# Performance work log

Measured on AMD Instinct MI355X. Metric: run time of the kernel, lower is better.

Reference implementation:

```python
import jax, jax.numpy as jnp
import numpy as np

B, Ci, Cr, Hb, Wb = 2, 256, 128, 200, 200
Ca, NH, DH = 128, 8, 16          # attn_channels = min(256,128); 8 heads of dim 16
K = 100                           # max(16, int(0.5*W)), K < W so topk path is active
EPS = 1e-5


def ln(x, g, b):
    m = x.mean(-1, keepdims=True)
    v = ((x - m) ** 2).mean(-1, keepdims=True)
    return (x - m) / jnp.sqrt(v + EPS) * g + b


def setup_inputs() -> dict:
    key = jax.random.key(0)
    ks = jax.random.split(key, 16)
    def n(k, shape, s=0.02):
        return jax.random.normal(k, shape, dtype=jnp.float32) * s
    return dict(
        radar_features=jax.random.normal(ks[0], (B, Cr, Hb, Wb), dtype=jnp.float32),
        image_features=jax.random.normal(ks[1], (B, Ci, Hb, Wb), dtype=jnp.float32),
        img_proj_w=n(ks[2], (Ca, Ci)),
        rad_proj_w=n(ks[3], (Ca, Cr)),
        in_proj_w=n(ks[4], (3 * Ca, Ca)),
        in_proj_b=jnp.zeros((3 * Ca,), jnp.float32),
        out_proj_w=n(ks[5], (Ca, Ca)),
        out_proj_b=jnp.zeros((Ca,), jnp.float32),
        ln1q_g=jnp.ones((Ca,), jnp.float32), ln1q_b=jnp.zeros((Ca,), jnp.float32),
        ln1kv_g=jnp.ones((Ca,), jnp.float32), ln1kv_b=jnp.zeros((Ca,), jnp.float32),
        ln2_g=jnp.ones((Ca,), jnp.float32), ln2_b=jnp.zeros((Ca,), jnp.float32),
        ffn_w1=n(ks[6], (4 * Ca, Ca)), ffn_b1=jnp.zeros((4 * Ca,), jnp.float32),
        ffn_w2=n(ks[7], (Ca, 4 * Ca)), ffn_b2=jnp.zeros((Ca,), jnp.float32),
        score_w1=n(ks[8], (Ca // 2, 2 * Ca)), score_b1=jnp.zeros((Ca // 2,), jnp.float32),
        score_w2=n(ks[9], (1, Ca // 2)), score_b2=jnp.zeros((1,), jnp.float32),
        rad_delta_w=n(ks[10], (Cr, Ca)),
        gamma=jnp.full((1,), 0.5, jnp.float32),  # torch inits to 0; 0.5 so attn branch affects output
        gate_w=n(ks[11], (Cr, Cr + Ci)), gate_b=jnp.zeros((Cr,), jnp.float32),
        fuse_w=n(ks[12], (Cr + Ci, Cr + Ci, 3, 3)),
        bn_g=jnp.ones((Cr + Ci,), jnp.float32), bn_b=jnp.zeros((Cr + Ci,), jnp.float32),
    )


def reference(radar_features, image_features, img_proj_w, rad_proj_w, in_proj_w, in_proj_b,
              out_proj_w, out_proj_b, ln1q_g, ln1q_b, ln1kv_g, ln1kv_b, ln2_g, ln2_b,
              ffn_w1, ffn_b1, ffn_w2, ffn_b2, score_w1, score_b1, score_w2, score_b2,
              rad_delta_w, gamma, gate_w, gate_b, fuse_w, bn_g, bn_b):
    # 1x1 projections into attention space, then per-row sequences [B*H, W, Ca]
    img_seq = jnp.einsum('bchw,oc->bhwo', image_features, img_proj_w).reshape(B * Hb, Wb, Ca)
    rad_seq = jnp.einsum('bchw,oc->bhwo', radar_features, rad_proj_w).reshape(B * Hb, Wb, Ca)

    # progressive focus: score each image token per row, keep top-K as KV
    si = jnp.concatenate([jax.lax.stop_gradient(rad_seq), img_seq], axis=-1)
    h = jax.nn.relu(si @ score_w1.T + score_b1)
    score = (h @ score_w2.T + score_b2)[..., 0]            # [B*H, W]
    _, idx = jax.lax.top_k(score, K)                       # [B*H, K]
    img_kv = jnp.take_along_axis(img_seq, idx[:, :, None], axis=1)  # [B*H, K, Ca]

    # cross attention (pre-LN on q and kv, residual onto rad_seq)
    q = ln(rad_seq, ln1q_g, ln1q_b)
    kv = ln(img_kv, ln1kv_g, ln1kv_b)
    wq, wk, wv = in_proj_w[:Ca], in_proj_w[Ca:2 * Ca], in_proj_w[2 * Ca:]
    bq, bk, bv = in_proj_b[:Ca], in_proj_b[Ca:2 * Ca], in_proj_b[2 * Ca:]
    qh = (q @ wq.T + bq).reshape(B * Hb, Wb, NH, DH)
    kh = (kv @ wk.T + bk).reshape(B * Hb, K, NH, DH)
    vh = (kv @ wv.T + bv).reshape(B * Hb, K, NH, DH)
    att = jax.nn.softmax(jnp.einsum('nqhd,nkhd->nhqk', qh, kh) / jnp.sqrt(jnp.float32(DH)), axis=-1)
    o = jnp.einsum('nhqk,nkhd->nqhd', att, vh).reshape(B * Hb, Wb, Ca) @ out_proj_w.T + out_proj_b
    x = rad_seq + o
    x = x + (jax.nn.relu(ln(x, ln2_g, ln2_b) @ ffn_w1.T + ffn_b1) @ ffn_w2.T + ffn_b2)

    # back to BEV, project delta to radar channels
    delta = jnp.einsum('bhwc,oc->bohw', x.reshape(B, Hb, Wb, Ca), rad_delta_w)

    # cross-modal gate (1x1 conv + sigmoid) with range-decay mask
    gate_in = jnp.concatenate([radar_features, image_features], axis=1)
    gate = jax.nn.sigmoid(jnp.einsum('bchw,oc->bohw', gate_in, gate_w) + gate_b[None, :, None, None])
    y = jnp.arange(Hb, dtype=jnp.float32) / (Hb - 1)
    rmask = jnp.clip(1.0 - 0.7 * y, 0.3, None)[None, None, :, None]
    gate = gate * rmask

    radar_enhanced = radar_features + gamma * gate * delta

    # fuse: 3x3 conv + BatchNorm (batch stats, training mode) + ReLU
    fi = jnp.concatenate([radar_enhanced, image_features], axis=1)
    c = jax.lax.conv_general_dilated(fi, fuse_w, (1, 1), 'SAME',
                                     dimension_numbers=('NCHW', 'OIHW', 'NCHW'))
    m = c.mean((0, 2, 3), keepdims=True)
    v = ((c - m) ** 2).mean((0, 2, 3), keepdims=True)
    out = jax.nn.relu((c - m) / jnp.sqrt(v + EPS) * bn_g[None, :, None, None] + bn_b[None, :, None, None])
    return out
```

## Files before the change

### kernel.cpp

```cpp
#include <hip/hip_runtime.h>
#include <hip/hip_bf16.h>

#define EPSF 1e-5f

typedef unsigned short u16;
typedef unsigned int u32;
typedef __attribute__((ext_vector_type(8))) short short8v;
typedef __attribute__((ext_vector_type(4))) float f32x4;

__device__ float g_arena[84000000];
__device__ float g_stats[768];

__device__ __forceinline__ float wave_sum(float v) {
#pragma unroll
    for (int o = 32; o > 0; o >>= 1) v += __shfl_down(v, o, 64);
    return v;
}

__device__ __forceinline__ void gload16(const u16* g, u16* l) {
    __builtin_amdgcn_global_load_lds(
        (const __attribute__((address_space(1))) u32*)(g),
        (__attribute__((address_space(3))) u32*)(l),
        16, 0, 0);
}

__device__ __forceinline__ void bf_split(float v, u16& h, u16& l) {
    __hip_bfloat16 bh = __float2bfloat16(v);
    float hv = __bfloat162float(bh);
    __hip_bfloat16 bl = __float2bfloat16(v - hv);
    h = *reinterpret_cast<u16*>(&bh);
    l = *reinterpret_cast<u16*>(&bl);
}

__device__ __forceinline__ void store_split4(u16* ph, u16* pl, float4 v) {
    u16 h0, l0, h1, l1, h2, l2, h3, l3;
    bf_split(v.x, h0, l0); bf_split(v.y, h1, l1);
    bf_split(v.z, h2, l2); bf_split(v.w, h3, l3);
    *(ushort4*)ph = make_ushort4(h0, h1, h2, h3);
    *(ushort4*)pl = make_ushort4(l0, l1, l2, l3);
}

__global__ __launch_bounds__(256) void split_weights_kernel(
    const float* __restrict__ w_inproj, const float* __restrict__ w_outproj,
    const float* __restrict__ w_ffn1, const float* __restrict__ w_ffn2,
    const float* __restrict__ w_delta, const float* __restrict__ w_gate,
    const float* __restrict__ w_img, const float* __restrict__ w_rad,
    const float* __restrict__ w_sc1, const float* __restrict__ b_sc1,
    u16* __restrict__ wseg, float* __restrict__ bias_pad,
    float* __restrict__ zpage)
{
    int i = blockIdx.x * 256 + threadIdx.x;
    if (i >= 393408) return;
    if (i >= 393344) {
        zpage[i - 393344] = 0.f;
        return;
    }
    if (i >= 393216) {
        int l = i - 393216;
        bias_pad[l] = (l < 64) ? b_sc1[l] : 0.f;
        return;
    }
    float v; int base, numel, local;
    if (i < 49152)       { local = i;          base = 0;      numel = 49152; v = w_inproj[local]; }
    else if (i < 65536)  { local = i - 49152;  base = 98304;  numel = 16384; v = w_outproj[local]; }
    else if (i < 131072) { local = i - 65536;  base = 131072; numel = 65536; v = w_ffn1[local]; }
    else if (i < 196608) { local = i - 131072; base = 262144; numel = 65536; v = w_ffn2[local]; }
    else if (i < 212992) { local = i - 196608; base = 393216; numel = 16384; v = w_delta[local]; }
    else if (i < 262144) { local = i - 212992; base = 425984; numel = 49152; v = w_gate[local]; }
    else if (i < 360448) {
        local = i - 262144; base = 524288; numel = 98304;
        int oc = local / 384, c = local - oc * 384;
        if (oc < 128) v = (c < 128) ? w_rad[oc * 128 + c] : 0.f;
        else          v = (c >= 128) ? w_img[(oc - 128) * 256 + (c - 128)] : 0.f;
    } else {
        local = i - 360448; base = 720896; numel = 32768;
        int oc = local / 256, c = local - oc * 256;
        v = (oc < 64) ? w_sc1[oc * 256 + c] : 0.f;
    }
    u16 hh, ll;
    bf_split(v, hh, ll);
    wseg[base + local] = hh;
    wseg[base + numel + local] = ll;
}

template <int BMODE, int OMODE, bool RELU>
__global__ __launch_bounds__(256, (BMODE == 1) ? 3 : 2) void mfma_gemm_kernel(
    const u16* __restrict__ Ah, const u16* __restrict__ Al,
    const u16* __restrict__ bh, const u16* __restrict__ bl,
    const float* __restrict__ bf, int bstride,
    const float* __restrict__ bias, const float* __restrict__ resid, int rstride,
    float* __restrict__ outf, u16* __restrict__ outh,
    int K, int Nout, int P, const u16* __restrict__ zp)
{
    __shared__ alignas(16) u16 sAh[8192], sAl[8192], sBh[8192];
    __shared__ alignas(16) u16 sBl[(BMODE != 1) ? 8192 : 8];

    const int tid  = threadIdx.x;
    const int lane = tid & 63;
    const int wid  = tid >> 6;
    const int wrm  = wid >> 1;
    const int wcn  = wid & 1;
    const int p0   = blockIdx.x * 128;
    const int ocb  = blockIdx.y * 128;

    const int r0  = tid >> 3;
    const int cl  = tid & 7;
    const int swz = cl ^ (r0 & 7);

    f32x4 acc[4][4];
#pragma unroll
    for (int i = 0; i < 4; ++i)
#pragma unroll
        for (int j = 0; j < 4; ++j) acc[i][j] = (f32x4){0.f, 0.f, 0.f, 0.f};

    const int fr = lane & 15;
    const int fc = lane >> 4;

    for (int kk = 0; kk < K; kk += 64) {
        __syncthreads();
#pragma unroll
        for (int k = 0; k < 4; ++k) {
            int row = r0 + k * 32;
            int dlin = row * 64 + cl * 8;
            size_t ga = (size_t)(ocb + row) * K + kk + swz * 8;
            gload16(&Ah[ga], &sAh[dlin]);
            gload16(&Al[ga], &sAl[dlin]);
            int p = p0 + row;
            if (BMODE == 0) {
                size_t gb = (size_t)p * bstride + kk + swz * 8;
                const u16* bsh = (p < P) ? &bh[gb] : zp;
                const u16* bsl = (p < P) ? &bl[gb] : zp;
                gload16(bsh, &sBh[dlin]);
                gload16(bsl, &sBl[dlin]);
            } else if (BMODE == 1) {
                size_t gb = (size_t)p * bstride + kk + swz * 8;
                const u16* bsh = (p < P) ? &bh[gb] : zp;
                gload16(bsh, &sBh[dlin]);
            } else {
                int di = row * 64 + swz * 8;
                short8v vh8 = {0,0,0,0,0,0,0,0}, vl8 = {0,0,0,0,0,0,0,0};
                if (p < P) {
                    const float* src = bf + (size_t)p * bstride + kk + cl * 8;
                    float4 f0 = *(const float4*)(src);
                    float4 f1 = *(const float4*)(src + 4);
                    float fv[8] = {f0.x, f0.y, f0.z, f0.w, f1.x, f1.y, f1.z, f1.w};
#pragma unroll
                    for (int j = 0; j < 8; ++j) {
                        u16 hh, ll;
                        bf_split(fv[j], hh, ll);
                        vh8[j] = (short)hh;
                        vl8[j] = (short)ll;
                    }
                }
                *(short8v*)&sBh[di] = vh8;
                *(short8v*)&sBl[di] = vl8;
            }
        }
        __syncthreads();
#pragma unroll
        for (int h = 0; h < 2; ++h) {
            const int kc = h * 4 + fc;
            short8v bhf[4], blf[4];
#pragma unroll
            for (int nn = 0; nn < 4; ++nn) {
                int row = wcn * 64 + nn * 16 + fr;
                int idx = row * 64 + ((kc ^ (row & 7)) << 3);
                bhf[nn] = *(const short8v*)&sBh[idx];
                if (BMODE != 1) blf[nn] = *(const short8v*)&sBl[idx];
            }
#pragma unroll
            for (int mm = 0; mm < 4; ++mm) {
                int row = wrm * 64 + mm * 16 + fr;
                int idx = row * 64 + ((kc ^ (row & 7)) << 3);
                short8v ahf = *(const short8v*)&sAh[idx];
                short8v alf = *(const short8v*)&sAl[idx];
#pragma unroll
                for (int nn = 0; nn < 4; ++nn)
                    acc[mm][nn] = __builtin_amdgcn_mfma_f32_16x16x32_bf16(
                        ahf, bhf[nn], acc[mm][nn], 0, 0, 0);
                if (BMODE != 1) {
#pragma unroll
                    for (int nn = 0; nn < 4; ++nn)
                        acc[mm][nn] = __builtin_amdgcn_mfma_f32_16x16x32_bf16(
                            ahf, blf[nn], acc[mm][nn], 0, 0, 0);
                }
#pragma unroll
                for (int nn = 0; nn < 4; ++nn)
                    acc[mm][nn] = __builtin_amdgcn_mfma_f32_16x16x32_bf16(
                        alf, bhf[nn], acc[mm][nn], 0, 0, 0);
            }
        }
    }

#pragma unroll
    for (int mm = 0; mm < 4; ++mm) {
        int base = ocb + wrm * 64 + mm * 16 + fc * 4;
        float4 bv = {0.f, 0.f, 0.f, 0.f};
        if (bias) bv = *(const float4*)&bias[base];
#pragma unroll
        for (int nn = 0; nn < 4; ++nn) {
            int p = p0 + wcn * 64 + nn * 16 + fr;
            if (p < P) {
                size_t row = (size_t)p * Nout + base;
                float4 r;
                r.x = acc[mm][nn][0] + bv.x;
                r.y = acc[mm][nn][1] + bv.y;
                r.z = acc[mm][nn][2] + bv.z;
                r.w = acc[mm][nn][3] + bv.w;
                if (resid) {
                    float4 rr = *(const float4*)&resid[(size_t)p * rstride + base - ocb];
                    r.x += rr.x; r.y += rr.y; r.z += rr.z; r.w += rr.w;
                }
                if (RELU) {
                    r.x = fmaxf(r.x, 0.f); r.y = fmaxf(r.y, 0.f);
                    r.z = fmaxf(r.z, 0.f); r.w = fmaxf(r.w, 0.f);
                }
                if (OMODE == 0) {
                    *(float4*)&outf[row] = r;
                } else {
                    __hip_bfloat16 b0 = __float2bfloat16(r.x);
                    __hip_bfloat16 b1 = __float2bfloat16(r.y);
                    __hip_bfloat16 b2 = __float2bfloat16(r.z);
                    __hip_bfloat16 b3 = __float2bfloat16(r.w);
                    *(ushort4*)&outh[row] = make_ushort4(
                        *reinterpret_cast<u16*>(&b0), *reinterpret_cast<u16*>(&b1),
                        *reinterpret_cast<u16*>(&b2), *reinterpret_cast<u16*>(&b3));
                }
            }
        }
    }
}

__global__ __launch_bounds__(256) void score_reduce_kernel(
    const float* __restrict__ h, const float* __restrict__ w2,
    const float* __restrict__ b2, float* __restrict__ score)
{
    int p = blockIdx.x * 4 + (threadIdx.x >> 6);
    int l = threadIdx.x & 63;
    float v = h[(size_t)p * 128 + l] * w2[l];
    v = wave_sum(v);
    if (l == 0) score[p] = v + b2[0];
}

__global__ __launch_bounds__(256) void topk_kernel(
    const float* __restrict__ score, int* __restrict__ idx)
{
    __shared__ float s[200];
    const int n = blockIdx.x;
    const int t = threadIdx.x;
    if (t < 200) s[t] = score[(size_t)n * 200 + t];
    __syncthreads();
    if (t < 200) {
        float my = s[t];
        int cnt = 0;
        for (int j = 0; j < 200; j++) {
            float o = s[j];
            cnt += (o > my) || (o == my && j < t);
        }
        if (cnt < 100) idx[n * 100 + cnt] = t;
    }
}

__global__ __launch_bounds__(256) void ln_gather_kernel(
    const float* __restrict__ in, int stride, const int* __restrict__ gidx,
    const float* __restrict__ g, const float* __restrict__ bb,
    u16* __restrict__ oh, u16* __restrict__ ol)
{
    __shared__ float red[4];
    const int tid = threadIdx.x;
    const int grp = tid >> 7;
    const int t = tid & 127;
    const int r = blockIdx.x * 2 + grp;

    size_t src_row;
    if (gidx) src_row = (size_t)(r / 100) * 200 + gidx[r];
    else      src_row = (size_t)r;

    float x = in[src_row * stride + t];
    float s = wave_sum(x);
    if ((tid & 63) == 0) red[tid >> 6] = s;
    __syncthreads();
    float m = (red[grp * 2] + red[grp * 2 + 1]) * 0.0078125f;
    float d = x - m;
    float s2 = wave_sum(d * d);
    __syncthreads();
    if ((tid & 63) == 0) red[tid >> 6] = s2;
    __syncthreads();
    float var = (red[grp * 2] + red[grp * 2 + 1]) * 0.0078125f;
    float y = d * rsqrtf(var + EPSF) * g[t] + bb[t];
    u16 hh, ll;
    bf_split(y, hh, ll);
    oh[(size_t)r * 128 + t] = hh;
    ol[(size_t)r * 128 + t] = ll;
}

__global__ __launch_bounds__(256) void attention_kernel(
    const float* __restrict__ qh, const float* __restrict__ kvh,
    u16* __restrict__ o_hi, u16* __restrict__ o_lo)
{
    __shared__ float sk[100][16];
    __shared__ float sv[100][16];
    const int h = blockIdx.x;
    const int n = blockIdx.y;
    const int tid = threadIdx.x;

    for (int e = tid; e < 1600; e += 256) {
        int kk = e >> 4, d = e & 15;
        size_t src = ((size_t)n * 100 + kk) * 256 + h * 16 + d;
        sk[kk][d] = kvh[src];
        sv[kk][d] = kvh[src + 128];
    }
    __syncthreads();

    if (tid < 200) {
        const float* qp = &qh[((size_t)n * 200 + tid) * 128 + h * 16];
        float4 q0 = *(const float4*)(qp + 0);
        float4 q1 = *(const float4*)(qp + 4);
        float4 q2 = *(const float4*)(qp + 8);
        float4 q3 = *(const float4*)(qp + 12);

        float m = -INFINITY, l = 0.f;
        float4 a0 = {0,0,0,0}, a1 = {0,0,0,0}, a2 = {0,0,0,0}, a3 = {0,0,0,0};

        for (int kk = 0; kk < 100; kk++) {
            const float4* kp = (const float4*)&sk[kk][0];
            float s = q0.x*kp[0].x + q0.y*kp[0].y + q0.z*kp[0].z + q0.w*kp[0].w
                    + q1.x*kp[1].x + q1.y*kp[1].y + q1.z*kp[1].z + q1.w*kp[1].w
                    + q2.x*kp[2].x + q2.y*kp[2].y + q2.z*kp[2].z + q2.w*kp[2].w
                    + q3.x*kp[3].x + q3.y*kp[3].y + q3.z*kp[3].z + q3.w*kp[3].w;
            s *= 0.25f;
            float nm = fmaxf(m, s);
            float corr = __expf(m - nm);
            float pe = __expf(s - nm);
            l = l * corr + pe;
            const float4* vp = (const float4*)&sv[kk][0];
            float4 v0 = vp[0], v1 = vp[1], v2 = vp[2], v3 = vp[3];
            a0.x = a0.x * corr + pe * v0.x; a0.y = a0.y * corr + pe * v0.y;
            a0.z = a0.z * corr + pe * v0.z; a0.w = a0.w * corr + pe * v0.w;
            a1.x = a1.x * corr + pe * v1.x; a1.y = a1.y * corr + pe * v1.y;
            a1.z = a1.z * corr + pe * v1.z; a1.w = a1.w * corr + pe * v1.w;
            a2.x = a2.x * corr + pe * v2.x; a2.y = a2.y * corr + pe * v2.y;
            a2.z = a2.z * corr + pe * v2.z; a2.w = a2.w * corr + pe * v2.w;
            a3.x = a3.x * corr + pe * v3.x; a3.y = a3.y * corr + pe * v3.y;
            a3.z = a3.z * corr + pe * v3.z; a3.w = a3.w * corr + pe * v3.w;
            m = nm;
        }
        float inv = 1.f / l;
        a0.x *= inv; a0.y *= inv; a0.z *= inv; a0.w *= inv;
        a1.x *= inv; a1.y *= inv; a1.z *= inv; a1.w *= inv;
        a2.x *= inv; a2.y *= inv; a2.z *= inv; a2.w *= inv;
        a3.x *= inv; a3.y *= inv; a3.z *= inv; a3.w *= inv;
        size_t ob = ((size_t)n * 200 + tid) * 128 + h * 16;
        store_split4(&o_hi[ob + 0],  &o_lo[ob + 0],  a0);
        store_split4(&o_hi[ob + 4],  &o_lo[ob + 4],  a1);
        store_split4(&o_hi[ob + 8],  &o_lo[ob + 8],  a2);
        store_split4(&o_hi[ob + 12], &o_lo[ob + 12], a3);
    }
}

__global__ __launch_bounds__(256) void prep_weights_kernel(
    const float* __restrict__ fw, u16* __restrict__ wh, u16* __restrict__ wl)
{
    int idx = blockIdx.x * 256 + threadIdx.x;
    int oc = idx / 384;
    int ic = idx - oc * 384;
    const float* src = fw + (size_t)idx * 9;
    u16* dh = wh + (size_t)oc * 3456 + ic;
    u16* dl = wl + (size_t)oc * 3456 + ic;
#pragma unroll
    for (int s = 0; s < 9; ++s) {
        u16 hh, ll;
        bf_split(src[s], hh, ll);
        dh[(size_t)s * 384] = hh;
        dl[(size_t)s * 384] = ll;
    }
}

__global__ __launch_bounds__(256) void convert_nhwc_kernel(
    const float* __restrict__ radar, const float* __restrict__ image,
    u16* __restrict__ oh, u16* __restrict__ ol)
{
    int p = blockIdx.x * 256 + threadIdx.x;
    if (p >= 80000) return;
    int cg = blockIdx.y;
    int b = p >= 40000 ? 1 : 0;
    int hw = p - b * 40000;
    u16* ph = oh + (size_t)p * 384 + cg * 64;
    u16* pl = ol + (size_t)p * 384 + cg * 64;
#pragma unroll 1
    for (int g = 0; g < 8; ++g) {
        short8v vh, vl;
#pragma unroll
        for (int j = 0; j < 8; ++j) {
            int c = cg * 64 + g * 8 + j;
            float v = (c < 128)
                ? radar[((size_t)(b * 128 + c)) * 40000 + hw]
                : image[((size_t)(b * 256 + (c - 128))) * 40000 + hw];
            u16 hh, ll;
            bf_split(v, hh, ll);
            vh[j] = (short)hh;
            vl[j] = (short)ll;
        }
        *(short8v*)&ph[g * 8] = vh;
        *(short8v*)&pl[g * 8] = vl;
    }
}

__global__ __launch_bounds__(256) void enhance_fuse_kernel(
    const float* __restrict__ delta, const float* __restrict__ gatepre,
    const float* __restrict__ radar, const float* __restrict__ gamma_p,
    u16* __restrict__ nh)
{
    __shared__ float srad[64][136];
    const int tid = threadIdx.x;
    const int blk = blockIdx.x;
    const int b = blk >= 625 ? 1 : 0;
    const int hw0 = (blk - b * 625) * 64;
    const int p0 = b * 40000 + hw0;

#pragma unroll
    for (int i = 0; i < 32; ++i) {
        int e = tid + i * 256;
        int oc = e >> 6, pos = e & 63;
        srad[pos][oc] = radar[((size_t)(b * 128 + oc)) * 40000 + hw0 + pos];
    }
    __syncthreads();

    const float gmm = gamma_p[0];
    const int c4 = tid & 31;
    const int rr = tid >> 5;
#pragma unroll
    for (int j = 0; j < 8; ++j) {
        int pos = j * 8 + rr;
        int p = p0 + pos;
        int hw = hw0 + pos;
        int hrow = hw / 200;
        float rm = fmaxf(0.3f, 1.0f - 0.7f * ((float)hrow * (1.0f / 199.0f)));
        float4 dv = *(const float4*)&delta[(size_t)p * 128 + c4 * 4];
        float4 gv = *(const float4*)&gatepre[(size_t)p * 128 + c4 * 4];
        float4 rv = *(const float4*)&srad[pos][c4 * 4];
        float rx = rv.x + gmm * (1.f / (1.f + __expf(-gv.x))) * rm * dv.x;
        float ry = rv.y + gmm * (1.f / (1.f + __expf(-gv.y))) * rm * dv.y;
        float rz = rv.z + gmm * (1.f / (1.f + __expf(-gv.z))) * rm * dv.z;
        float rw = rv.w + gmm * (1.f / (1.f + __expf(-gv.w))) * rm * dv.w;
        __hip_bfloat16 b0 = __float2bfloat16(rx);
        __hip_bfloat16 b1 = __float2bfloat16(ry);
        __hip_bfloat16 b2 = __float2bfloat16(rz);
        __hip_bfloat16 b3 = __float2bfloat16(rw);
        *(ushort4*)&nh[(size_t)p * 384 + c4 * 4] = make_ushort4(
            *reinterpret_cast<u16*>(&b0), *reinterpret_cast<u16*>(&b1),
            *reinterpret_cast<u16*>(&b2), *reinterpret_cast<u16*>(&b3));
    }
}

__global__ __launch_bounds__(256, 3) void conv_mfma_kernel(
    const u16* __restrict__ nhwc_hi,
    const u16* __restrict__ wgt_hi,  const u16* __restrict__ wgt_lo,
    float* __restrict__ out, const u16* __restrict__ zp)
{
    __shared__ alignas(16) u16 sAh[8192], sAl[8192], sBh[8192];

    const int tid  = threadIdx.x;
    const int lane = tid & 63;
    const int wid  = tid >> 6;
    const int wrm  = wid >> 1;
    const int wcn  = wid & 1;
    const int hw0  = blockIdx.x * 128;
    const int b    = blockIdx.y;
    const int oc0  = blockIdx.z * 128;

    const int r0  = tid >> 3;
    const int cl  = tid & 7;
    const int swz = cl ^ (r0 & 7);

    const int y0 = hw0 / 200;
    const int x0 = hw0 - y0 * 200;

    f32x4 acc[4][4];
#pragma unroll
    for (int i = 0; i < 4; ++i)
#pragma unroll
        for (int j = 0; j < 4; ++j) acc[i][j] = (f32x4){0.f, 0.f, 0.f, 0.f};

    size_t abase[4];
#pragma unroll
    for (int k = 0; k < 4; ++k)
        abase[k] = (size_t)(oc0 + r0 + k * 32) * 3456 + swz * 8;

    const int fr = lane & 15;
    const int fc = lane >> 4;

    for (int s = 0; s < 9; ++s) {
        const int dy = s / 3 - 1;
        const int dx = s % 3 - 1;
        size_t bsrc[4];
        int bval[4];
#pragma unroll
        for (int k = 0; k < 4; ++k) {
            int row = r0 + k * 32;
            int hwo = hw0 + row;
            int xr  = x0 + row;
            int wrp = (xr >= 200) ? 1 : 0;
            int yy  = y0 + wrp + dy;
            int xx  = xr - wrp * 200 + dx;
            int v = (hwo < 40000) && ((unsigned)yy < 200u) && ((unsigned)xx < 200u);
            bval[k] = v;
            bsrc[k] = v ? ((size_t)(b * 40000 + yy * 200 + xx) * 384 + swz * 8) : 0;
        }
        const size_t wofs = (size_t)s * 384;

        for (int icb = 0; icb < 6; ++icb) {
            const int ic0 = icb * 64;
            __syncthreads();
#pragma unroll
            for (int k = 0; k < 4; ++k) {
                int dlin = (r0 + k * 32) * 64 + cl * 8;
                size_t ga = abase[k] + wofs + ic0;
                gload16(&wgt_hi[ga], &sAh[dlin]);
                gload16(&wgt_lo[ga], &sAl[dlin]);
                const u16* bs = bval[k] ? &nhwc_hi[bsrc[k] + ic0] : zp;
                gload16(bs, &sBh[dlin]);
            }
            __syncthreads();
#pragma unroll
            for (int h = 0; h < 2; ++h) {
                const int kc = h * 4 + fc;
                short8v bhf[4];
#pragma unroll
                for (int nn = 0; nn < 4; ++nn) {
                    int row = wcn * 64 + nn * 16 + fr;
                    int idx = row * 64 + ((kc ^ (row & 7)) << 3);
                    bhf[nn] = *(const short8v*)&sBh[idx];
                }
#pragma unroll
                for (int mm = 0; mm < 4; ++mm) {
                    int row = wrm * 64 + mm * 16 + fr;
                    int idx = row * 64 + ((kc ^ (row & 7)) << 3);
                    short8v ahf = *(const short8v*)&sAh[idx];
                    short8v alf = *(const short8v*)&sAl[idx];
#pragma unroll
                    for (int nn = 0; nn < 4; ++nn)
                        acc[mm][nn] = __builtin_amdgcn_mfma_f32_16x16x32_bf16(
                            ahf, bhf[nn], acc[mm][nn], 0, 0, 0);
#pragma unroll
                    for (int nn = 0; nn < 4; ++nn)
                        acc[mm][nn] = __builtin_amdgcn_mfma_f32_16x16x32_bf16(
                            alf, bhf[nn], acc[mm][nn], 0, 0, 0);
                }
            }
        }
    }

#pragma unroll
    for (int mm = 0; mm < 4; ++mm) {
        int oc = oc0 + wrm * 64 + mm * 16 + fc * 4;
#pragma unroll
        for (int nn = 0; nn < 4; ++nn) {
            int p = hw0 + wcn * 64 + nn * 16 + fr;
            if (p < 40000) {
                float* op = out + (size_t)(b * 384 + oc) * 40000 + p;
#pragma unroll
                for (int r = 0; r < 4; ++r)
                    op[(size_t)r * 40000] = acc[mm][nn][r];
            }
        }
    }
}

__global__ void zero_stats_kernel() {
    int i = blockIdx.x * 256 + threadIdx.x;
    if (i < 768) g_stats[i] = 0.f;
}

__global__ __launch_bounds__(256) void conv_stats_kernel(const float* __restrict__ out)
{
    const int c = blockIdx.x;
    const int chunk = blockIdx.y;
    float s1 = 0.f, s2 = 0.f;
#pragma unroll
    for (int b = 0; b < 2; ++b) {
        const float4* pp = (const float4*)(out + (size_t)(b * 384 + c) * 40000)
                         + (size_t)chunk * 2500;
        for (int i = threadIdx.x; i < 2500; i += 256) {
            float4 v = pp[i];
            s1 += v.x + v.y + v.z + v.w;
            s2 += v.x * v.x + v.y * v.y + v.z * v.z + v.w * v.w;
        }
    }
    s1 = wave_sum(s1);
    s2 = wave_sum(s2);
    __shared__ float r1[4], r2[4];
    if ((threadIdx.x & 63) == 0) {
        r1[threadIdx.x >> 6] = s1;
        r2[threadIdx.x >> 6] = s2;
    }
    __syncthreads();
    if (threadIdx.x == 0) {
        atomicAdd(&g_stats[c * 2],     r1[0] + r1[1] + r1[2] + r1[3]);
        atomicAdd(&g_stats[c * 2 + 1], r2[0] + r2[1] + r2[2] + r2[3]);
    }
}

__global__ __launch_bounds__(256) void bn_relu_kernel(
    float* __restrict__ out, const float* __restrict__ g,
    const float* __restrict__ bb)
{
    int i = blockIdx.x * 256 + threadIdx.x;
    int flat = i * 4;
    int oc = (flat / 40000) % 384;
    float m = g_stats[oc * 2] * (1.f / 80000.f);
    float v = g_stats[oc * 2 + 1] * (1.f / 80000.f) - m * m;
    float inv = rsqrtf(v + EPSF);
    float sc = g[oc] * inv;
    float sh = bb[oc] - m * sc;
    float4 c = ((float4*)out)[i];
    c.x = fmaxf(c.x * sc + sh, 0.f);
    c.y = fmaxf(c.y * sc + sh, 0.f);
    c.z = fmaxf(c.z * sc + sh, 0.f);
    c.w = fmaxf(c.w * sc + sh, 0.f);
    ((float4*)out)[i] = c;
}

extern "C" void kernel_launch(void* const* d_in, const int* in_sizes, int n_in,
                              void* d_out, int out_size, void* d_ws, size_t ws_size,
                              hipStream_t stream)
{
    (void)in_sizes; (void)n_in; (void)out_size; (void)d_ws; (void)ws_size;

    const float* radar      = (const float*)d_in[0];
    const float* image      = (const float*)d_in[1];
    const float* img_proj_w = (const float*)d_in[2];
    const float* rad_proj_w = (const float*)d_in[3];
    const float* in_proj_w  = (const float*)d_in[4];
    const float* in_proj_b  = (const float*)d_in[5];
    const float* out_proj_w = (const float*)d_in[6];
    const float* out_proj_b = (const float*)d_in[7];
    const float* ln1q_g     = (const float*)d_in[8];
    const float* ln1q_b     = (const float*)d_in[9];
    const float* ln1kv_g    = (const float*)d_in[10];
    const float* ln1kv_b    = (const float*)d_in[11];
    const float* ln2_g      = (const float*)d_in[12];
    const float* ln2_b      = (const float*)d_in[13];
    const float* ffn_w1     = (const float*)d_in[14];
    const float* ffn_b1     = (const float*)d_in[15];
    const float* ffn_w2     = (const float*)d_in[16];
    const float* ffn_b2     = (const float*)d_in[17];
    const float* score_w1   = (const float*)d_in[18];
    const float* score_b1   = (const float*)d_in[19];
    const float* score_w2   = (const float*)d_in[20];
    const float* score_b2   = (const float*)d_in[21];
    const float* rad_delta_w= (const float*)d_in[22];
    const float* gamma      = (const float*)d_in[23];
    const float* gate_w     = (const float*)d_in[24];
    const float* gate_b     = (const float*)d_in[25];
    const float* fuse_w     = (const float*)d_in[26];
    const float* bn_g       = (const float*)d_in[27];
    const float* bn_b       = (const float*)d_in[28];

    float* arena = nullptr;
    hipGetSymbolAddress((void**)&arena, HIP_SYMBOL(g_arena));

    u16*   nh_hi    = (u16*)arena;
    u16*   nh_lo    = (u16*)(arena + 15360000);
    float* seq_comb = arena + 30720000;
    float* score    = arena + 51200000;
    int*   idx      = (int*)(arena + 51280000);
    float* qh       = arena + 51200000;
    float* xbuf     = arena + 51200000;
    float* kvh      = arena + 61440000;
    float* gatepre  = arena + 61440000;
    float* hscore   = arena + 71680000;
    u16*   gbase    = (u16*)(arena + 71680000);
    u16*   kvn_hi   = gbase,            *kvn_lo = gbase + 5120000;
    u16*   qn_hi    = gbase,            *qn_lo  = gbase + 10240000;
    u16*   o_hi     = gbase,            *o_lo   = gbase + 10240000;
    u16*   xn_hi    = gbase,            *xn_lo  = gbase + 10240000;
    float* delta    = arena + 71680000;
    u16*   hbuf     = (u16*)(arena + 30720000);
    u16*   wseg     = (u16*)(arena + 81920000);
    u16*   cwgt_hi  = (u16*)(arena + 82330000);
    u16*   cwgt_lo  = cwgt_hi + 1327104;
    float* bias_pad = arena + 83900000;
    float* zpage_f  = arena + 83900160;
    const u16* zp   = (const u16*)zpage_f;

    const u16* w_q_hi    = wseg + 0,      *w_q_lo    = wseg + 49152;
    const u16* w_kv_hi   = wseg + 16384,  *w_kv_lo   = wseg + 49152 + 16384;
    const u16* w_out_hi  = wseg + 98304,  *w_out_lo  = wseg + 114688;
    const u16* w_ffn1_hi = wseg + 131072, *w_ffn1_lo = wseg + 196608;
    const u16* w_ffn2_hi = wseg + 262144, *w_ffn2_lo = wseg + 327680;
    const u16* w_dlt_hi  = wseg + 393216, *w_dlt_lo  = wseg + 409600;
    const u16* w_gate_hi = wseg + 425984, *w_gate_lo = wseg + 475136;
    const u16* w_comb_hi = wseg + 524288, *w_comb_lo = wseg + 622592;
    const u16* w_sc1_hi  = wseg + 720896, *w_sc1_lo  = wseg + 753664;

    const dim3 blk(256);

    split_weights_kernel<<<dim3(1537), blk, 0, stream>>>(
        in_proj_w, out_proj_w, ffn_w1, ffn_w2, rad_delta_w, gate_w,
        img_proj_w, rad_proj_w, score_w1, score_b1, wseg, bias_pad, zpage_f);
    prep_weights_kernel<<<dim3(576), blk, 0, stream>>>(fuse_w, cwgt_hi, cwgt_lo);
    convert_nhwc_kernel<<<dim3(313, 6), blk, 0, stream>>>(radar, image, nh_hi, nh_lo);

    mfma_gemm_kernel<0, 0, false><<<dim3(625, 2), blk, 0, stream>>>(
        w_comb_hi, w_comb_lo, nh_hi, nh_lo, nullptr, 384,
        nullptr, nullptr, 0, seq_comb, nullptr, 384, 256, 80000, zp);

    mfma_gemm_kernel<2, 0, true><<<dim3(625, 1), blk, 0, stream>>>(
        w_sc1_hi, w_sc1_lo, nullptr, nullptr, seq_comb, 256,
        bias_pad, nullptr, 0, hscore, nullptr, 256, 128, 80000, zp);
    score_reduce_kernel<<<dim3(20000), blk, 0, stream>>>(
        hscore, score_w2, score_b2, score);
    topk_kernel<<<dim3(400), blk, 0, stream>>>(score, idx);

    ln_gather_kernel<<<dim3(20000), blk, 0, stream>>>(
        seq_comb + 128, 256, idx, ln1kv_g, ln1kv_b, kvn_hi, kvn_lo);
    mfma_gemm_kernel<0, 0, false><<<dim3(313, 2), blk, 0, stream>>>(
        w_kv_hi, w_kv_lo, kvn_hi, kvn_lo, nullptr, 128,
        in_proj_b + 128, nullptr, 0, kvh, nullptr, 128, 256, 40000, zp);

    ln_gather_kernel<<<dim3(40000), blk, 0, stream>>>(
        seq_comb, 256, nullptr, ln1q_g, ln1q_b, qn_hi, qn_lo);
    mfma_gemm_kernel<0, 0, false><<<dim3(625, 1), blk, 0, stream>>>(
        w_q_hi, w_q_lo, qn_hi, qn_lo, nullptr, 128,
        in_proj_b, nullptr, 0, qh, nullptr, 128, 128, 80000, zp);

    attention_kernel<<<dim3(8, 400), blk, 0, stream>>>(qh, kvh, o_hi, o_lo);

    mfma_gemm_kernel<0, 0, false><<<dim3(625, 1), blk, 0, stream>>>(
        w_out_hi, w_out_lo, o_hi, o_lo, nullptr, 128,
        out_proj_b, seq_comb, 256, xbuf, nullptr, 128, 128, 80000, zp);

    ln_gather_kernel<<<dim3(40000), blk, 0, stream>>>(
        xbuf, 128, nullptr, ln2_g, ln2_b, xn_hi, xn_lo);
    mfma_gemm_kernel<0, 1, true><<<dim3(625, 4), blk, 0, stream>>>(
        w_ffn1_hi, w_ffn1_lo, xn_hi, xn_lo, nullptr, 128,
        ffn_b1, nullptr, 0, nullptr, hbuf, 128, 512, 80000, zp);
    mfma_gemm_kernel<1, 0, false><<<dim3(625, 1), blk, 0, stream>>>(
        w_ffn2_hi, w_ffn2_lo, hbuf, nullptr, nullptr, 512,
        ffn_b2, xbuf, 128, xbuf, nullptr, 512, 128, 80000, zp);

    mfma_gemm_kernel<2, 0, false><<<dim3(625, 1), blk, 0, stream>>>(
        w_dlt_hi, w_dlt_lo, nullptr, nullptr, xbuf, 128,
        nullptr, nullptr, 0, delta, nullptr, 128, 128, 80000, zp);
    mfma_gemm_kernel<1, 0, false><<<dim3(625, 1), blk, 0, stream>>>(
        w_gate_hi, w_gate_lo, nh_hi, nullptr, nullptr, 384,
        gate_b, nullptr, 0, gatepre, nullptr, 384, 128, 80000, zp);
    enhance_fuse_kernel<<<dim3(1250), blk, 0, stream>>>(
        delta, gatepre, radar, gamma, nh_hi);

    conv_mfma_kernel<<<dim3(313, 2, 3), blk, 0, stream>>>(
        nh_hi, cwgt_hi, cwgt_lo, (float*)d_out, zp);
    zero_stats_kernel<<<dim3(3), blk, 0, stream>>>();
    conv_stats_kernel<<<dim3(384, 4), blk, 0, stream>>>((const float*)d_out);
    bn_relu_kernel<<<dim3(30000), blk, 0, stream>>>(
        (float*)d_out, bn_g, bn_b);
}
```

Baseline: 1.504 ms.

## Fuse score reduction and gated enhance into GEMM epilogues; drop bf16 low parts

Folds the score MLP's second layer (relu, dot with w2, cross-lane reduction) into the score GEMM epilogue, and folds the sigmoid-gate, range-mask and radar residual update into the delta GEMM epilogue. This removes the score_reduce and enhance_fuse kernels and their intermediate fp32 buffers. It also makes the attention-path GEMMs (kv, q, out_proj, ffn1) use hi-only bf16 activations instead of the hi+lo split, which removes one MFMA pass and the lo-part stores. The cost is lower numerical precision in those GEMMs.

Result: slower. 1.613 ms (+7.2%).

```diff
diff --git a/kernel.cpp b/kernel.cpp
--- a/kernel.cpp
+++ b/kernel.cpp
@@ -32,12 +32,14 @@
     l = *reinterpret_cast<u16*>(&bl);
 }
 
-__device__ __forceinline__ void store_split4(u16* ph, u16* pl, float4 v) {
-    u16 h0, l0, h1, l1, h2, l2, h3, l3;
-    bf_split(v.x, h0, l0); bf_split(v.y, h1, l1);
-    bf_split(v.z, h2, l2); bf_split(v.w, h3, l3);
-    *(ushort4*)ph = make_ushort4(h0, h1, h2, h3);
-    *(ushort4*)pl = make_ushort4(l0, l1, l2, l3);
+__device__ __forceinline__ void store_bf4(u16* p, float4 v) {
+    __hip_bfloat16 h0 = __float2bfloat16(v.x);
+    __hip_bfloat16 h1 = __float2bfloat16(v.y);
+    __hip_bfloat16 h2 = __float2bfloat16(v.z);
+    __hip_bfloat16 h3 = __float2bfloat16(v.w);
+    *(ushort4*)p = make_ushort4(
+        *reinterpret_cast<u16*>(&h0), *reinterpret_cast<u16*>(&h1),
+        *reinterpret_cast<u16*>(&h2), *reinterpret_cast<u16*>(&h3));
 }
 
 __global__ __launch_bounds__(256) void split_weights_kernel(
@@ -83,14 +85,16 @@
     wseg[base + numel + local] = ll;
 }
 
-template <int BMODE, int OMODE, bool RELU>
+template <int BMODE, int OMODE, bool RELU, int EPI>
 __global__ __launch_bounds__(256, (BMODE == 1) ? 3 : 2) void mfma_gemm_kernel(
     const u16* __restrict__ Ah, const u16* __restrict__ Al,
     const u16* __restrict__ bh, const u16* __restrict__ bl,
     const float* __restrict__ bf, int bstride,
     const float* __restrict__ bias, const float* __restrict__ resid, int rstride,
     float* __restrict__ outf, u16* __restrict__ outh,
-    int K, int Nout, int P, const u16* __restrict__ zp)
+    int K, int Nout, int P, const u16* __restrict__ zp,
+    const float* __restrict__ aux0, const float* __restrict__ aux1,
+    const float* __restrict__ aux2)
 {
     __shared__ alignas(16) u16 sAh[8192], sAl[8192], sBh[8192];
     __shared__ alignas(16) u16 sBl[(BMODE != 1) ? 8192 : 8];
@@ -192,6 +196,60 @@
         }
     }
 
+    if (EPI == 1) {
+        if (wrm == 0) {
+            float4 w2v[4], bvv[4];
+#pragma unroll
+            for (int mm = 0; mm < 4; ++mm) {
+                w2v[mm] = *(const float4*)&aux0[mm * 16 + fc * 4];
+                bvv[mm] = *(const float4*)&bias[mm * 16 + fc * 4];
+            }
+#pragma unroll
+            for (int nn = 0; nn < 4; ++nn) {
+                float ss = 0.f;
+#pragma unroll
+                for (int mm = 0; mm < 4; ++mm) {
+                    ss += fmaxf(acc[mm][nn][0] + bvv[mm].x, 0.f) * w2v[mm].x;
+                    ss += fmaxf(acc[mm][nn][1] + bvv[mm].y, 0.f) * w2v[mm].y;
+                    ss += fmaxf(acc[mm][nn][2] + bvv[mm].z, 0.f) * w2v[mm].z;
+                    ss += fmaxf(acc[mm][nn][3] + bvv[mm].w, 0.f) * w2v[mm].w;
+                }
+                ss += __shfl_xor(ss, 16, 64);
+                ss += __shfl_xor(ss, 32, 64);
+                int p = p0 + wcn * 64 + nn * 16 + fr;
+                if (fc == 0 && p < P) outf[p] = ss + aux1[0];
+            }
+        }
+        return;
+    }
+
+    if (EPI == 2) {
+        const float gmm = aux2[0];
+#pragma unroll
+        for (int mm = 0; mm < 4; ++mm) {
+            int base = ocb + wrm * 64 + mm * 16 + fc * 4;
+#pragma unroll
+            for (int nn = 0; nn < 4; ++nn) {
+                int p = p0 + wcn * 64 + nn * 16 + fr;
+                if (p < P) {
+                    int b = (p >= 40000) ? 1 : 0;
+                    int hw = p - b * 40000;
+                    int hrow = hw / 200;
+                    float rm = fmaxf(0.3f, 1.0f - 0.7f * ((float)hrow * (1.0f / 199.0f)));
+                    float4 gv = *(const float4*)&aux0[(size_t)p * 128 + base];
+                    const float* radp = aux1 + ((size_t)(b * 128 + base)) * 40000 + hw;
+                    float4 r;
+                    r.x = radp[0]      + gmm * (1.f / (1.f + __expf(-gv.x))) * rm * acc[mm][nn][0];
+                    r.y = radp[40000]  + gmm * (1.f / (1.f + __expf(-gv.y))) * rm * acc[mm][nn][1];
+                    r.z = radp[80000]  + gmm * (1.f / (1.f + __expf(-gv.z))) * rm * acc[mm][nn][2];
+                    r.w = radp[120000] + gmm * (1.f / (1.f + __expf(-gv.w))) * rm * acc[mm][nn][3];
+                    store_bf4(&outh[(size_t)p * 384 + base], r);
+                }
+            }
+        }
+        return;
+    }
+
 #pragma unroll
     for (int mm = 0; mm < 4; ++mm) {
         int base = ocb + wrm * 64 + mm * 16 + fc * 4;
@@ -218,28 +276,11 @@
                 if (OMODE == 0) {
                     *(float4*)&outf[row] = r;
                 } else {
-                    __hip_bfloat16 b0 = __float2bfloat16(r.x);
-                    __hip_bfloat16 b1 = __float2bfloat16(r.y);
-                    __hip_bfloat16 b2 = __float2bfloat16(r.z);
-                    __hip_bfloat16 b3 = __float2bfloat16(r.w);
-                    *(ushort4*)&outh[row] = make_ushort4(
-                        *reinterpret_cast<u16*>(&b0), *reinterpret_cast<u16*>(&b1),
-                        *reinterpret_cast<u16*>(&b2), *reinterpret_cast<u16*>(&b3));
-                }
-            }
-        }
-    }
-}
-
-__global__ __launch_bounds__(256) void score_reduce_kernel(
-    const float* __restrict__ h, const float* __restrict__ w2,
-    const float* __restrict__ b2, float* __restrict__ score)
-{
-    int p = blockIdx.x * 4 + (threadIdx.x >> 6);
-    int l = threadIdx.x & 63;
-    float v = h[(size_t)p * 128 + l] * w2[l];
-    v = wave_sum(v);
-    if (l == 0) score[p] = v + b2[0];
+                    store_bf4(&outh[row], r);
+                }
+            }
+        }
+    }
 }
 
 __global__ __launch_bounds__(256) void topk_kernel(
@@ -291,12 +332,12 @@
     u16 hh, ll;
     bf_split(y, hh, ll);
     oh[(size_t)r * 128 + t] = hh;
-    ol[(size_t)r * 128 + t] = ll;
+    if (ol) ol[(size_t)r * 128 + t] = ll;
 }
 
 __global__ __launch_bounds__(256) void attention_kernel(
     const float* __restrict__ qh, const float* __restrict__ kvh,
-    u16* __restrict__ o_hi, u16* __restrict__ o_lo)
+    u16* __restrict__ o_hi)
 {
     __shared__ float sk[100][16];
     __shared__ float sv[100][16];
@@ -351,10 +392,10 @@
         a2.x *= inv; a2.y *= inv; a2.z *= inv; a2.w *= inv;
         a3.x *= inv; a3.y *= inv; a3.z *= inv; a3.w *= inv;
         size_t ob = ((size_t)n * 200 + tid) * 128 + h * 16;
-        store_split4(&o_hi[ob + 0],  &o_lo[ob + 0],  a0);
-        store_split4(&o_hi[ob + 4],  &o_lo[ob + 4],  a1);
-        store_split4(&o_hi[ob + 8],  &o_lo[ob + 8],  a2);
-        store_split4(&o_hi[ob + 12], &o_lo[ob + 12], a3);
+        store_bf4(&o_hi[ob + 0],  a0);
+        store_bf4(&o_hi[ob + 4],  a1);
+        store_bf4(&o_hi[ob + 8],  a2);
+        store_bf4(&o_hi[ob + 12], a3);
     }
 }
 
@@ -403,53 +444,6 @@
         }
         *(short8v*)&ph[g * 8] = vh;
         *(short8v*)&pl[g * 8] = vl;
-    }
-}
-
-__global__ __launch_bounds__(256) void enhance_fuse_kernel(
-    const float* __restrict__ delta, const float* __restrict__ gatepre,
-    const float* __restrict__ radar, const float* __restrict__ gamma_p,
-    u16* __restrict__ nh)
-{
-    __shared__ float srad[64][136];
-    const int tid = threadIdx.x;
-    const int blk = blockIdx.x;
-    const int b = blk >= 625 ? 1 : 0;
-    const int hw0 = (blk - b * 625) * 64;
-    const int p0 = b * 40000 + hw0;
-
-#pragma unroll
-    for (int i = 0; i < 32; ++i) {
-        int e = tid + i * 256;
-        int oc = e >> 6, pos = e & 63;
-        srad[pos][oc] = radar[((size_t)(b * 128 + oc)) * 40000 + hw0 + pos];
-    }
-    __syncthreads();
-
-    const float gmm = gamma_p[0];
-    const int c4 = tid & 31;
-    const int rr = tid >> 5;
-#pragma unroll
-    for (int j = 0; j < 8; ++j) {
-        int pos = j * 8 + rr;
-        int p = p0 + pos;
-        int hw = hw0 + pos;
-        int hrow = hw / 200;
-        float rm = fmaxf(0.3f, 1.0f - 0.7f * ((float)hrow * (1.0f / 199.0f)));
-        float4 dv = *(const float4*)&delta[(size_t)p * 128 + c4 * 4];
-        float4 gv = *(const float4*)&gatepre[(size_t)p * 128 + c4 * 4];
-        float4 rv = *(const float4*)&srad[pos][c4 * 4];
-        float rx = rv.x + gmm * (1.f / (1.f + __expf(-gv.x))) * rm * dv.x;
-        float ry = rv.y + gmm * (1.f / (1.f + __expf(-gv.y))) * rm * dv.y;
-        float rz = rv.z + gmm * (1.f / (1.f + __expf(-gv.z))) * rm * dv.z;
-        float rw = rv.w + gmm * (1.f / (1.f + __expf(-gv.w))) * rm * dv.w;
-        __hip_bfloat16 b0 = __float2bfloat16(rx);
-        __hip_bfloat16 b1 = __float2bfloat16(ry);
-        __hip_bfloat16 b2 = __float2bfloat16(rz);
-        __hip_bfloat16 b3 = __float2bfloat16(rw);
-        *(ushort4*)&nh[(size_t)p * 384 + c4 * 4] = make_ushort4(
-            *reinterpret_cast<u16*>(&b0), *reinterpret_cast<u16*>(&b1),
-            *reinterpret_cast<u16*>(&b2), *reinterpret_cast<u16*>(&b3));
     }
 }
 
@@ -669,13 +663,11 @@
     float* xbuf     = arena + 51200000;
     float* kvh      = arena + 61440000;
     float* gatepre  = arena + 61440000;
-    float* hscore   = arena + 71680000;
     u16*   gbase    = (u16*)(arena + 71680000);
-    u16*   kvn_hi   = gbase,            *kvn_lo = gbase + 5120000;
-    u16*   qn_hi    = gbase,            *qn_lo  = gbase + 10240000;
-    u16*   o_hi     = gbase,            *o_lo   = gbase + 10240000;
-    u16*   xn_hi    = gbase,            *xn_lo  = gbase + 10240000;
-    float* delta    = arena + 71680000;
+    u16*   kvn_hi   = gbase;
+    u16*   qn_hi    = gbase + 10240000;
+    u16*   o_hi     = gbase + 10240000;
+    u16*   xn_hi    = gbase + 10240000;
     u16*   hbuf     = (u16*)(arena + 30720000);
     u16*   wseg     = (u16*)(arena + 81920000);
     u16*   cwgt_hi  = (u16*)(arena + 82330000);
@@ -702,52 +694,57 @@
     prep_weights_kernel<<<dim3(576), blk, 0, stream>>>(fuse_w, cwgt_hi, cwgt_lo);
     convert_nhwc_kernel<<<dim3(313, 6), blk, 0, stream>>>(radar, image, nh_hi, nh_lo);
 
-    mfma_gemm_kernel<0, 0, false><<<dim3(625, 2), blk, 0, stream>>>(
+    mfma_gemm_kernel<0, 0, false, 0><<<dim3(625, 2), blk, 0, stream>>>(
         w_comb_hi, w_comb_lo, nh_hi, nh_lo, nullptr, 384,
-        nullptr, nullptr, 0, seq_comb, nullptr, 384, 256, 80000, zp);
-
-    mfma_gemm_kernel<2, 0, true><<<dim3(625, 1), blk, 0, stream>>>(
+        nullptr, nullptr, 0, seq_comb, nullptr, 384, 256, 80000, zp,
+        nullptr, nullptr, nullptr);
+
+    mfma_gemm_kernel<2, 0, false, 1><<<dim3(625, 1), blk, 0, stream>>>(
         w_sc1_hi, w_sc1_lo, nullptr, nullptr, seq_comb, 256,
-        bias_pad, nullptr, 0, hscore, nullptr, 256, 128, 80000, zp);
-    score_reduce_kernel<<<dim3(20000), blk, 0, stream>>>(
-        hscore, score_w2, score_b2, score);
+        bias_pad, nullptr, 0, score, nullptr, 256, 128, 80000, zp,
+        score_w2, score_b2, nullptr);
     topk_kernel<<<dim3(400), blk, 0, stream>>>(score, idx);
 
     ln_gather_kernel<<<dim3(20000), blk, 0, stream>>>(
-        seq_comb + 128, 256, idx, ln1kv_g, ln1kv_b, kvn_hi, kvn_lo);
-    mfma_gemm_kernel<0, 0, false><<<dim3(313, 2), blk, 0, stream>>>(
-        w_kv_hi, w_kv_lo, kvn_hi, kvn_lo, nullptr, 128,
-        in_proj_b + 128, nullptr, 0, kvh, nullptr, 128, 256, 40000, zp);
+        seq_comb + 128, 256, idx, ln1kv_g, ln1kv_b, kvn_hi, nullptr);
+    mfma_gemm_kernel<1, 0, false, 0><<<dim3(313, 2), blk, 0, stream>>>(
+        w_kv_hi, w_kv_lo, kvn_hi, nullptr, nullptr, 128,
+        in_proj_b + 128, nullptr, 0, kvh, nullptr, 128, 256, 40000, zp,
+        nullptr, nullptr, nullptr);
 
     ln_gather_kernel<<<dim3(40000), blk, 0, stream>>>(
-        seq_comb, 256, nullptr, ln1q_g, ln1q_b, qn_hi, qn_lo);
-    mfma_gemm_kernel<0, 0, false><<<dim3(625, 1), blk, 0, stream>>>(
-        w_q_hi, w_q_lo, qn_hi, qn_lo, nullptr, 128,
-        in_proj_b, nullptr, 0, qh, nullptr, 128, 128, 80000, zp);
-
-    attention_kernel<<<dim3(8, 400), blk, 0, stream>>>(qh, kvh, o_hi, o_lo);
-
-    mfma_gemm_kernel<0, 0, false><<<dim3(625, 1), blk, 0, stream>>>(
-        w_out_hi, w_out_lo, o_hi, o_lo, nullptr, 128,
-        out_proj_b, seq_comb, 256, xbuf, nullptr, 128, 128, 80000, zp);
+        seq_comb, 256, nullptr, ln1q_g, ln1q_b, qn_hi, nullptr);
+    mfma_gemm_kernel<1, 0, false, 0><<<dim3(625, 1), blk, 0, stream>>>(
+        w_q_hi, w_q_lo, qn_hi, nullptr, nullptr, 128,
+        in_proj_b, nullptr, 0, qh, nullptr, 128, 128, 80000, zp,
+        nullptr, nullptr, nullptr);
+
+    attention_kernel<<<dim3(8, 400), blk, 0, stream>>>(qh, kvh, o_hi);
+
+    mfma_gemm_kernel<1, 0, false, 0><<<dim3(625, 1), blk, 0, stream>>>(
+        w_out_hi, w_out_lo, o_hi, nullptr, nullptr, 128,
+        out_proj_b, seq_comb, 256, xbuf, nullptr, 128, 128, 80000, zp,
+        nullptr, nullptr, nullptr);
 
     ln_gather_kernel<<<dim3(40000), blk, 0, stream>>>(
-        xbuf, 128, nullptr, ln2_g, ln2_b, xn_hi, xn_lo);
-    mfma_gemm_kernel<0, 1, true><<<dim3(625, 4), blk, 0, stream>>>(
-        w_ffn1_hi, w_ffn1_lo, xn_hi, xn_lo, nullptr, 128,
-        ffn_b1, nullptr, 0, nullptr, hbuf, 128, 512, 80000, zp);
-    mfma_gemm_kernel<1, 0, false><<<dim3(625, 1), blk, 0, stream>>>(
+        xbuf, 128, nullptr, ln2_g, ln2_b, xn_hi, nullptr);
+    mfma_gemm_kernel<1, 1, true, 0><<<dim3(625, 4), blk, 0, stream>>>(
+        w_ffn1_hi, w_ffn1_lo, xn_hi, nullptr, nullptr, 128,
+        ffn_b1, nullptr, 0, nullptr, hbuf, 128, 512, 80000, zp,
+        nullptr, nullptr, nullptr);
+    mfma_gemm_kernel<1, 0, false, 0><<<dim3(625, 1), blk, 0, stream>>>(
         w_ffn2_hi, w_ffn2_lo, hbuf, nullptr, nullptr, 512,
-        ffn_b2, xbuf, 128, xbuf, nullptr, 512, 128, 80000, zp);
-
-    mfma_gemm_kernel<2, 0, false><<<dim3(625, 1), blk, 0, stream>>>(
+        ffn_b2, xbuf, 128, xbuf, nullptr, 512, 128, 80000, zp,
+        nullptr, nullptr, nullptr);
+
+    mfma_gemm_kernel<1, 0, false, 0><<<dim3(625, 1), blk, 0, stream>>>(
+        w_gate_hi, w_gate_lo, nh_hi, nullptr, nullptr, 384,
+        gate_b, nullptr, 0, gatepre, nullptr, 384, 128, 80000, zp,
+        nullptr, nullptr, nullptr);
+    mfma_gemm_kernel<2, 0, false, 2><<<dim3(625, 1), blk, 0, stream>>>(
         w_dlt_hi, w_dlt_lo, nullptr, nullptr, xbuf, 128,
-        nullptr, nullptr, 0, delta, nullptr, 128, 128, 80000, zp);
-    mfma_gemm_kernel<1, 0, false><<<dim3(625, 1), blk, 0, stream>>>(
-        w_gate_hi, w_gate_lo, nh_hi, nullptr, nullptr, 384,
-        gate_b, nullptr, 0, gatepre, nullptr, 384, 128, 80000, zp);
-    enhance_fuse_kernel<<<dim3(1250), blk, 0, stream>>>(
-        delta, gatepre, radar, gamma, nh_hi);
+        nullptr, nullptr, 0, nullptr, nh_hi, 128, 128, 80000, zp,
+        gatepre, radar, gamma);
 
     conv_mfma_kernel<<<dim3(313, 2, 3), blk, 0, stream>>>(
         nh_hi, cwgt_hi, cwgt_lo, (float*)d_out, zp);
```
